# Performance work log

Measured on AMD Instinct MI355X. Metric: run time of the kernel, lower is better.

Reference implementation:

```python
import jax, jax.numpy as jnp
import numpy as np

# Static group structure: B groups, each of uniform size N, feature dim C.
# (The torch module handles ragged groups with a Python loop; with uniform
# groups the pad-to-max step is an identity and the math below is exact.)
B, N, C = 512, 64, 1024
EPS = 1e-12  # F.normalize default eps


def setup_inputs() -> dict:
    key = jax.random.key(0)
    feats = jax.random.normal(key, (B * N, C), dtype=jnp.float32)
    # adjacent equal labels: group g occupies rows [g*N, (g+1)*N)
    labels = jnp.repeat(jnp.arange(B, dtype=jnp.int32), N)
    return {"feats": feats, "labels": labels}


def reference(feats, labels):
    # labels encode contiguous uniform groups of size N (see setup_inputs),
    # so grouping is a static reshape.
    g = feats.reshape(B, N, C)                                  # [B, N, C]
    # F.normalize(dim=1): row-wise L2 normalize with eps clamp
    norms = jnp.linalg.norm(g, axis=-1, keepdims=True)
    gn = g / jnp.maximum(norms, EPS)
    # per-group cosine-similarity matrix and mean relation score
    sim = jnp.einsum('bnc,bmc->bnm', gn, gn)                    # [B, N, N]
    rel = sim.mean(axis=2)                                      # [B, N]
    # argsort descending (torch.argsort(..., descending=True))
    order = jnp.argsort(-rel, axis=1)                           # [B, N]
    sorted_g = jnp.take_along_axis(g, order[:, :, None], axis=1)
    out_sorted = sorted_g.reshape(B, N * C)                     # [B, N*C]
    out_input = g.reshape(B, N * C)                             # input-order concat (training=True)
    return out_sorted, out_input
```

## Files before the change

### kernel.cpp

```cpp
#include <hip/hip_runtime.h>
#include <math.h>


constexpr int Bq = 512;
constexpr int Nq = 64;
constexpr int Cq = 1024;
constexpr int C4 = Cq / 4;
constexpr int G4 = Nq * C4;
constexpr int OUT_HALF4 = Bq * G4;

__global__ __launch_bounds__(256)
void group_sorter_kernel(const float* __restrict__ feats, float* __restrict__ out) {
    __shared__ float  s_lds[Cq];
    __shared__ double rnorm[Nq];
    __shared__ double rel[Nq];
    __shared__ int    dst_row[Nq];

    const int b    = blockIdx.x;
    const int t    = threadIdx.x;
    const int wave = t >> 6;
    const int lane = t & 63;

    const float4* __restrict__ g4 =
        reinterpret_cast<const float4*>(feats) + (size_t)b * G4;

    for (int n = wave; n < Nq; n += 4) {
        const float4* row = g4 + n * C4;
        double acc = 0.0;
        #pragma unroll
        for (int j = 0; j < 4; ++j) {
            float4 v = row[lane + 64 * j];
            acc += (double)v.x * v.x + (double)v.y * v.y
                 + (double)v.z * v.z + (double)v.w * v.w;
        }
        #pragma unroll
        for (int off = 32; off > 0; off >>= 1) acc += __shfl_xor(acc, off, 64);
        if (lane == 0) rnorm[n] = 1.0 / fmax(sqrt(acc), 1e-12);
    }
    __syncthreads();

    {
        double s0 = 0, s1 = 0, s2 = 0, s3 = 0;
        for (int m = 0; m < Nq; ++m) {
            float4 v = g4[m * C4 + t];
            double rn = rnorm[m];
            s0 += (double)v.x * rn; s1 += (double)v.y * rn;
            s2 += (double)v.z * rn; s3 += (double)v.w * rn;
        }
        reinterpret_cast<float4*>(s_lds)[t] =
            make_float4((float)s0, (float)s1, (float)s2, (float)s3);
    }
    __syncthreads();

    {
        const float4* s4 = reinterpret_cast<const float4*>(s_lds);
        for (int n = wave; n < Nq; n += 4) {
            const float4* row = g4 + n * C4;
            double acc = 0.0;
            #pragma unroll
            for (int j = 0; j < 4; ++j) {
                float4 v  = row[lane + 64 * j];
                float4 sv = s4[lane + 64 * j];
                acc += (double)v.x * sv.x + (double)v.y * sv.y
                     + (double)v.z * sv.z + (double)v.w * sv.w;
            }
            #pragma unroll
            for (int off = 32; off > 0; off >>= 1) acc += __shfl_xor(acc, off, 64);
            if (lane == 0) rel[n] = acc * rnorm[n];
        }
    }
    __syncthreads();

    if (t < Nq) {
        double mine = rel[t];
        int r = 0;
        for (int m = 0; m < Nq; ++m) {
            double o = rel[m];
            r += (o > mine) || (o == mine && m < t);
        }
        dst_row[t] = r;
    }
    __syncthreads();

    float4* os = reinterpret_cast<float4*>(out) + (size_t)b * G4;
    float4* oi = reinterpret_cast<float4*>(out) + OUT_HALF4 + (size_t)b * G4;
    for (int i = 0; i < Nq; ++i) {
        int f = i * C4 + t;
        float4 v = g4[f];
        oi[f] = v;
        os[dst_row[i] * C4 + t] = v;
    }
}

extern "C" void kernel_launch(void* const* d_in, const int* in_sizes, int n_in,
                              void* d_out, int out_size, void* d_ws, size_t ws_size,
                              hipStream_t stream) {
    const float* feats = (const float*)d_in[0];
    float* out = (float*)d_out;
    hipLaunchKernelGGL(group_sorter_kernel, dim3(Bq), dim3(256), 0, stream,
                       feats, out);
}
```

Before: 407.5 us.

## Use 1024-thread blocks, split column-sum over row parts, fuse input-copy store

Raises the block size from 256 to 1024 threads so 16 waves per group share the norm, column-sum and dot-product phases. The column-sum is split into four row partitions whose partial sums are reduced through shared memory. The input-order copy is moved into the column-sum pass, which removes one global reread of the group. Both output halves are now written with nontemporal stores. The larger block raises per-block shared memory and register pressure, which may limit how many blocks fit on each CU.

```diff
diff --git a/kernel.cpp b/kernel.cpp
--- a/kernel.cpp
+++ b/kernel.cpp
@@ -9,8 +9,11 @@
 constexpr int G4 = Nq * C4;
 constexpr int OUT_HALF4 = Bq * G4;
 
-__global__ __launch_bounds__(256)
+typedef float f4 __attribute__((ext_vector_type(4)));
+
+__global__ __launch_bounds__(1024)
 void group_sorter_kernel(const float* __restrict__ feats, float* __restrict__ out) {
+    __shared__ double sp[4][C4][4];
     __shared__ float  s_lds[Cq];
     __shared__ double rnorm[Nq];
     __shared__ double rel[Nq];
@@ -21,15 +24,16 @@
     const int wave = t >> 6;
     const int lane = t & 63;
 
-    const float4* __restrict__ g4 =
-        reinterpret_cast<const float4*>(feats) + (size_t)b * G4;
+    const f4* __restrict__ g4 = reinterpret_cast<const f4*>(feats) + (size_t)b * G4;
+    f4* __restrict__ os = reinterpret_cast<f4*>(out) + (size_t)b * G4;
+    f4* __restrict__ oi = reinterpret_cast<f4*>(out) + OUT_HALF4 + (size_t)b * G4;
 
-    for (int n = wave; n < Nq; n += 4) {
-        const float4* row = g4 + n * C4;
+    for (int n = wave; n < Nq; n += 16) {
+        const f4* row = g4 + n * C4;
         double acc = 0.0;
         #pragma unroll
         for (int j = 0; j < 4; ++j) {
-            float4 v = row[lane + 64 * j];
+            f4 v = row[lane + 64 * j];
             acc += (double)v.x * v.x + (double)v.y * v.y
                  + (double)v.z * v.z + (double)v.w * v.w;
         }
@@ -40,27 +44,39 @@
     __syncthreads();
 
     {
+        const int part = t >> 8;
+        const int c4   = t & 255;
         double s0 = 0, s1 = 0, s2 = 0, s3 = 0;
-        for (int m = 0; m < Nq; ++m) {
-            float4 v = g4[m * C4 + t];
+        #pragma unroll 4
+        for (int mm = 0; mm < 16; ++mm) {
+            const int m = part * 16 + mm;
+            f4 v = g4[m * C4 + c4];
             double rn = rnorm[m];
             s0 += (double)v.x * rn; s1 += (double)v.y * rn;
             s2 += (double)v.z * rn; s3 += (double)v.w * rn;
+            __builtin_nontemporal_store(v, &oi[m * C4 + c4]);
         }
-        reinterpret_cast<float4*>(s_lds)[t] =
-            make_float4((float)s0, (float)s1, (float)s2, (float)s3);
+        sp[part][c4][0] = s0; sp[part][c4][1] = s1;
+        sp[part][c4][2] = s2; sp[part][c4][3] = s3;
+    }
+    __syncthreads();
+    {
+        const int c4 = t >> 2, comp = t & 3;
+        double sum = sp[0][c4][comp] + sp[1][c4][comp]
+                   + sp[2][c4][comp] + sp[3][c4][comp];
+        s_lds[c4 * 4 + comp] = (float)sum;
     }
     __syncthreads();
 
     {
-        const float4* s4 = reinterpret_cast<const float4*>(s_lds);
-        for (int n = wave; n < Nq; n += 4) {
-            const float4* row = g4 + n * C4;
+        const f4* s4 = reinterpret_cast<const f4*>(s_lds);
+        for (int n = wave; n < Nq; n += 16) {
+            const f4* row = g4 + n * C4;
             double acc = 0.0;
             #pragma unroll
             for (int j = 0; j < 4; ++j) {
-                float4 v  = row[lane + 64 * j];
-                float4 sv = s4[lane + 64 * j];
+                f4 v  = row[lane + 64 * j];
+                f4 sv = s4[lane + 64 * j];
                 acc += (double)v.x * sv.x + (double)v.y * sv.y
                      + (double)v.z * sv.z + (double)v.w * sv.w;
             }
@@ -82,13 +98,15 @@
     }
     __syncthreads();
 
-    float4* os = reinterpret_cast<float4*>(out) + (size_t)b * G4;
-    float4* oi = reinterpret_cast<float4*>(out) + OUT_HALF4 + (size_t)b * G4;
-    for (int i = 0; i < Nq; ++i) {
-        int f = i * C4 + t;
-        float4 v = g4[f];
-        oi[f] = v;
-        os[dst_row[i] * C4 + t] = v;
+    {
+        const int rsub = t >> 8;
+        const int c4   = t & 255;
+        #pragma unroll 4
+        for (int i4 = 0; i4 < 16; ++i4) {
+            const int i = i4 * 4 + rsub;
+            f4 v = g4[i * C4 + c4];
+            __builtin_nontemporal_store(v, &os[dst_row[i] * C4 + c4]);
+        }
     }
 }
 
@@ -97,6 +115,6 @@
                               hipStream_t stream) {
     const float* feats = (const float*)d_in[0];
     float* out = (float*)d_out;
-    hipLaunchKernelGGL(group_sorter_kernel, dim3(Bq), dim3(256), 0, stream,
+    hipLaunchKernelGGL(group_sorter_kernel, dim3(Bq), dim3(1024), 0, stream,
                        feats, out);
 }
```

Result: faster. 398.0 us (-2.3%).
